# Performance work log

Measured on AMD Instinct MI355X. Metric: run time of the kernel, lower is better.

Reference implementation:

```python
import jax, jax.numpy as jnp
import numpy as np

B, N, F_IN, H, E, C = 64, 1024, 128, 128, 1048576, 6
RATIO = 0.5
N1 = int(N * RATIO)        # nodes per graph after pool1 = 512
N2 = int(N1 * RATIO)       # nodes per graph after pool2 = 256


def setup_inputs() -> dict:
    key = jax.random.key(0)
    ks = jax.random.split(key, 14)
    x = jax.random.normal(ks[0], (B * N, F_IN), jnp.float32)
    # edges constrained within each graph (uniform graph size N)
    src = jax.random.randint(ks[1], (E,), 0, B * N, dtype=jnp.int32)
    dst = (src // N) * N + jax.random.randint(ks[2], (E,), 0, N, dtype=jnp.int32)
    edge_index = jnp.stack([src, dst]).astype(jnp.int64)
    batch = jnp.repeat(jnp.arange(B, dtype=jnp.int64), N)

    def lin(k, i, o):
        return (jax.random.normal(k, (i, o), jnp.float32) / np.sqrt(i)).astype(jnp.float32)

    W1 = lin(ks[3], F_IN, H); b1 = jnp.zeros((H,), jnp.float32)
    ws1 = jax.random.normal(ks[4], (H,), jnp.float32) / np.sqrt(H)
    W2 = lin(ks[5], H, H); b2 = jnp.zeros((H,), jnp.float32)
    ws2 = jax.random.normal(ks[6], (H,), jnp.float32) / np.sqrt(H)
    W3 = lin(ks[7], H, H); b3 = jnp.zeros((H,), jnp.float32)
    ws3 = jax.random.normal(ks[8], (H,), jnp.float32) / np.sqrt(H)
    L1w = lin(ks[9], 2 * H, H); L1b = jnp.zeros((H,), jnp.float32)
    L2w = lin(ks[10], H, H // 2); L2b = jnp.zeros((H // 2,), jnp.float32)
    L3w = lin(ks[11], H // 2, C); L3b = jnp.zeros((C,), jnp.float32)
    return dict(x=x, edge_index=edge_index, batch=batch,
                W1=W1, b1=b1, ws1=ws1, W2=W2, b2=b2, ws2=ws2, W3=W3, b3=b3, ws3=ws3,
                L1w=L1w, L1b=L1b, L2w=L2w, L2b=L2b, L3w=L3w, L3b=L3b)


def gcn_conv(x, src, dst, emask, W, b, ws, n_nodes):
    # GCNConv with self-loops: out_i = sum_j m_ij h_j / sqrt(d_i d_j) + h_i / d_i, d = deg+1
    h = x @ W
    deg = jax.ops.segment_sum(emask, dst, num_segments=n_nodes) + 1.0
    norm = emask / jnp.sqrt(deg[src] * deg[dst])                 # [E]
    agg = jax.ops.segment_sum(h[src] * norm[:, None], dst, num_segments=n_nodes)
    out = agg + h / deg[:, None] + b
    score = out @ ws                                             # [n] attention score
    return out, score


def att_pool(x, score, src, dst, emask, n_per_graph):
    # top-k node selection per graph (uniform sizes -> static shapes)
    k = int(n_per_graph * RATIO)
    vals, idx = jax.lax.top_k(score.reshape(B, n_per_graph), k)  # [B, k]
    gidx = (idx + (jnp.arange(B) * n_per_graph)[:, None]).reshape(-1)
    x_new = x[gidx] * jnp.tanh(vals.reshape(-1))[:, None]
    # remap old node ids -> new compact ids; drop edges touching removed nodes
    newpos = jnp.full((B * n_per_graph,), -1, jnp.int32).at[gidx].set(
        jnp.arange(B * k, dtype=jnp.int32))
    nsrc = newpos[src]; ndst = newpos[dst]
    nmask = emask * (nsrc >= 0) * (ndst >= 0)
    return x_new, jnp.maximum(nsrc, 0), jnp.maximum(ndst, 0), nmask, k


def readout(h, bvec, n_per_graph):
    gmp = jax.ops.segment_max(h, bvec, num_segments=B)
    gap = jax.ops.segment_sum(h, bvec, num_segments=B) / n_per_graph
    return jnp.concatenate([gmp, gap], axis=1)                   # [B, 2H]


def reference(x, edge_index, batch, W1, b1, ws1, W2, b2, ws2, W3, b3, ws3,
              L1w, L1b, L2w, L2b, L3w, L3b):
    src = edge_index[0].astype(jnp.int32)
    dst = edge_index[1].astype(jnp.int32)
    emask = jnp.ones((E,), x.dtype)

    h, s = gcn_conv(x, src, dst, emask, W1, b1, ws1, B * N)
    h = jax.nn.relu(h)
    h, src, dst, emask, k1 = att_pool(h, s, src, dst, emask, N)
    b1v = jnp.repeat(jnp.arange(B), k1)
    x1 = readout(h, b1v, float(k1))

    h, s = gcn_conv(h, src, dst, emask, W2, b2, ws2, B * k1)
    h = jax.nn.relu(h)
    h, src, dst, emask, k2 = att_pool(h, s, src, dst, emask, k1)
    b2v = jnp.repeat(jnp.arange(B), k2)
    x2 = readout(h, b2v, float(k2))

    h, s = gcn_conv(h, src, dst, emask, W3, b3, ws3, B * k2)
    h = jax.nn.relu(h)
    x3 = readout(h, b2v, float(k2))

    z = jax.nn.relu(x1) + jax.nn.relu(x2) + jax.nn.relu(x3)
    z = jax.nn.relu(z @ L1w + L1b)
    z = jax.nn.relu(z @ L2w + L2b)
    return jax.nn.log_softmax(z @ L3w + L3b, axis=-1)
```

## Files before the change

kernel.cpp:

```cpp
#include <hip/hip_runtime.h>
#include <math.h>

#define E_TOT 1048576
#define NB    64
#define HD    128
#define NN1   65536
#define NN2   32768
#define NN3   16384
#define CAP   18432
#define WST   140
#define PSTR  64
#define SMEM_PREP (2*16*128*4 + 2*16*WST*4)

__global__ void probe_kernel(const int* __restrict__ ei, int* __restrict__ flag,
                             int* __restrict__ gcur, int2* __restrict__ csr2) {
    int t = threadIdx.x;
    if (t < 64) { gcur[t] = 0; csr2[E_TOT + t] = make_int2(0, 0); }
    if (blockIdx.x == 0 && t == 0) {
        int w = 1;
        for (int i = 1; i < 64; i += 2) if (ei[i] != 0) { w = 0; break; }
        *flag = w;
    }
}

__device__ __forceinline__ void bin_pack_body(char* smem, const int* __restrict__ ei,
                                              const int* __restrict__ wflag,
                                              int* __restrict__ bins,
                                              int* __restrict__ gcur, int bid) {
    int* hist  = (int*)smem;
    int* base  = hist + 64;
    int* gpos  = base + 64;
    int* stage = gpos + 64;
    const int t = threadIdx.x;
    const int wide = *wflag;
    const int e0 = bid * 4096;
    const int2* ei2 = (const int2*)ei;

    int pk[16];
    #pragma unroll
    for (int j = 0; j < 16; ++j) {
        int e = e0 + j * 256 + t;
        int s, d;
        if (wide) { s = ei2[e].x; d = ei2[E_TOT + e].x; }
        else      { s = ei[e];    d = ei[E_TOT + e]; }
        int g = d >> 10;
        pk[j] = (g << 20) | ((d & 1023) << 10) | (s & 1023);
    }
    if (t < 64) hist[t] = 0;
    __syncthreads();
    #pragma unroll
    for (int j = 0; j < 16; ++j) atomicAdd(&hist[pk[j] >> 20], 1);
    __syncthreads();
    if (t < 64) {
        int v = hist[t];
        int inc = v;
        #pragma unroll
        for (int d = 1; d < 64; d <<= 1) { int u = __shfl_up(inc, d); if (t >= d) inc += u; }
        base[t] = inc - v;
        gpos[t] = atomicAdd(&gcur[t], v);
    }
    __syncthreads();
    if (t < 64) hist[t] = base[t];
    __syncthreads();
    #pragma unroll
    for (int j = 0; j < 16; ++j) {
        int p = atomicAdd(&hist[pk[j] >> 20], 1);
        stage[p] = pk[j];
    }
    __syncthreads();
    #pragma unroll
    for (int j = 0; j < 16; ++j) {
        int i = j * 256 + t;
        int v = stage[i];
        int g = v >> 20;
        int dst = gpos[g] + (i - base[g]);
        if (dst < CAP) bins[g * CAP + dst] = v;
    }
}

__device__ __forceinline__ void gemm_body(char* smem, const float* __restrict__ X,
                                          const int* __restrict__ sel,
                                          const float* __restrict__ scal,
                                          const float* __restrict__ W,
                                          float* __restrict__ Y, int bid) {
    float* sXT = (float*)smem;
    float* sW  = sXT + 2 * 16 * 128;
    const int t = threadIdx.x;
    const long long row0 = (long long)bid * 128;
    const int r0 = (t >> 4) << 3;
    const int c0 = (t & 15) << 3;
    const int wofs = c0 + ((c0 >> 5) << 2);
    const int lm  = t >> 1;
    const int lk  = (t & 1) << 3;
    const int wk  = t >> 4;
    const int wc8 = (t & 15) << 3;
    const int wpos = wc8 + ((wc8 >> 5) << 2);

    const float* xrow;
    float sc;
    if (sel) { xrow = X + (long long)sel[row0 + lm] * 128; sc = scal[row0 + lm]; }
    else     { xrow = X + (row0 + lm) * 128;               sc = 1.f; }

    float acc[8][8];
    #pragma unroll
    for (int i = 0; i < 8; ++i)
        #pragma unroll
        for (int j = 0; j < 8; ++j) acc[i][j] = 0.f;

    {
        float4 xa = *(const float4*)(xrow + lk);
        float4 xb = *(const float4*)(xrow + lk + 4);
        float4 wa = *(const float4*)(W + wk * 128 + wc8);
        float4 wb = *(const float4*)(W + wk * 128 + wc8 + 4);
        sXT[(lk + 0) * 128 + lm] = xa.x * sc; sXT[(lk + 1) * 128 + lm] = xa.y * sc;
        sXT[(lk + 2) * 128 + lm] = xa.z * sc; sXT[(lk + 3) * 128 + lm] = xa.w * sc;
        sXT[(lk + 4) * 128 + lm] = xb.x * sc; sXT[(lk + 5) * 128 + lm] = xb.y * sc;
        sXT[(lk + 6) * 128 + lm] = xb.z * sc; sXT[(lk + 7) * 128 + lm] = xb.w * sc;
        *(float4*)&sW[wk * WST + wpos]     = wa;
        *(float4*)&sW[wk * WST + wpos + 4] = wb;
    }
    int cur = 0;
    for (int k0 = 0; k0 < 128; k0 += 16) {
        __syncthreads();
        const bool hasNext = (k0 + 16) < 128;
        float4 nxa, nxb, nwa, nwb;
        if (hasNext) {
            nxa = *(const float4*)(xrow + k0 + 16 + lk);
            nxb = *(const float4*)(xrow + k0 + 16 + lk + 4);
            nwa = *(const float4*)(W + (k0 + 16 + wk) * 128 + wc8);
            nwb = *(const float4*)(W + (k0 + 16 + wk) * 128 + wc8 + 4);
        }
        #pragma unroll
        for (int kk = 0; kk < 16; ++kk) {
            float4 xa = *(const float4*)&sXT[(cur * 16 + kk) * 128 + r0];
            float4 xb = *(const float4*)&sXT[(cur * 16 + kk) * 128 + r0 + 4];
            float4 wa = *(const float4*)&sW[(cur * 16 + kk) * WST + wofs];
            float4 wb = *(const float4*)&sW[(cur * 16 + kk) * WST + wofs + 4];
            float xr[8]  = {xa.x, xa.y, xa.z, xa.w, xb.x, xb.y, xb.z, xb.w};
            float wcv[8] = {wa.x, wa.y, wa.z, wa.w, wb.x, wb.y, wb.z, wb.w};
            #pragma unroll
            for (int i = 0; i < 8; ++i)
                #pragma unroll
                for (int j = 0; j < 8; ++j)
                    acc[i][j] = fmaf(xr[i], wcv[j], acc[i][j]);
        }
        if (hasNext) {
            int nxt = cur ^ 1;
            sXT[(nxt * 16 + lk + 0) * 128 + lm] = nxa.x * sc;
            sXT[(nxt * 16 + lk + 1) * 128 + lm] = nxa.y * sc;
            sXT[(nxt * 16 + lk + 2) * 128 + lm] = nxa.z * sc;
            sXT[(nxt * 16 + lk + 3) * 128 + lm] = nxa.w * sc;
            sXT[(nxt * 16 + lk + 4) * 128 + lm] = nxb.x * sc;
            sXT[(nxt * 16 + lk + 5) * 128 + lm] = nxb.y * sc;
            sXT[(nxt * 16 + lk + 6) * 128 + lm] = nxb.z * sc;
            sXT[(nxt * 16 + lk + 7) * 128 + lm] = nxb.w * sc;
            *(float4*)&sW[(nxt * 16 + wk) * WST + wpos]     = nwa;
            *(float4*)&sW[(nxt * 16 + wk) * WST + wpos + 4] = nwb;
            cur = nxt;
        }
    }

    #pragma unroll
    for (int i = 0; i < 8; ++i) {
        float* yp = Y + (row0 + r0 + i) * 128 + c0;
        float4 o0; o0.x = acc[i][0]; o0.y = acc[i][1]; o0.z = acc[i][2]; o0.w = acc[i][3];
        float4 o1; o1.x = acc[i][4]; o1.y = acc[i][5]; o1.z = acc[i][6]; o1.w = acc[i][7];
        *(float4*)yp       = o0;
        *(float4*)(yp + 4) = o1;
    }
}

__device__ __forceinline__ void csr_build_body(const int2* __restrict__ old_off2,
                                               const int* __restrict__ old_deg,
                                               const int* __restrict__ old_csr,
                                               int old_stride,
                                               const int* __restrict__ map,
                                               const int* __restrict__ sel,
                                               int* __restrict__ new_csr,
                                               int* __restrict__ deg,
                                               float* __restrict__ rs,
                                               int nnew, int wid, int lane) {
    if (wid >= nnew) return;
    int old = sel[wid];
    int beg, end;
    if (old_off2) { int2 oe = old_off2[old]; beg = oe.x; end = oe.y; }
    else          { beg = old * PSTR; end = beg + old_deg[old]; }
    int out = wid * PSTR;
    int total = 0;
    for (int base = beg; base < end; base += 64) {
        int i = base + lane;
        int ns = -1;
        if (i < end) ns = map[old_csr[i * old_stride]];
        unsigned long long b = __ballot(ns >= 0);
        int pos = __popcll(b & ((1ULL << lane) - 1));
        if (ns >= 0 && total + pos < PSTR) new_csr[out + total + pos] = ns;
        total += __popcll(b);
    }
    if (total > PSTR) total = PSTR;
    if (lane == 0) {
        deg[wid] = total;
        rs[wid]  = rsqrtf((float)(total + 1));
    }
}

__device__ __forceinline__ void readout_g_body(const float* __restrict__ h,
                                               const int* __restrict__ sel,
                                               const float* __restrict__ scal,
                                               float* __restrict__ part,
                                               int npg, int b, int f) {
    int g = b >> 3, c = b & 7;
    int chunk = npg >> 3;
    int i0 = g * npg + c * chunk;
    float m = -INFINITY, s = 0.f;
    for (int n = 0; n < chunk; ++n) {
        int idx = i0 + n;
        float v = h[(long long)sel[idx] * 128 + f] * scal[idx];
        m = fmaxf(m, v);
        s += v;
    }
    part[(size_t)b * 256 + f]       = m;
    part[(size_t)b * 256 + 128 + f] = s;
}

__global__ __launch_bounds__(256) void prep1_kernel(const int* __restrict__ ei,
                                                    const int* __restrict__ wflag,
                                                    int* __restrict__ bins,
                                                    int* __restrict__ gcur,
                                                    const float* __restrict__ X,
                                                    const float* __restrict__ W1,
                                                    float* __restrict__ A) {
    extern __shared__ __align__(16) char smem[];
    if (blockIdx.x < 256) bin_pack_body(smem, ei, wflag, bins, gcur, blockIdx.x);
    else                  gemm_body(smem, X, nullptr, nullptr, W1, A, blockIdx.x - 256);
}

__global__ __launch_bounds__(256) void stage_prep_kernel(
        const float* __restrict__ Bf, const int* __restrict__ sel,
        const float* __restrict__ scal, const float* __restrict__ W,
        float* __restrict__ A,
        const int2* __restrict__ old_off2, const int* __restrict__ old_deg,
        const int* __restrict__ old_csr, int old_stride,
        const int* __restrict__ map, int* __restrict__ new_csr,
        int* __restrict__ deg, float* __restrict__ rs, int nnew,
        float* __restrict__ part, int npg, int ngemm, int ncsr) {
    extern __shared__ __align__(16) char smem[];
    int b = blockIdx.x;
    if (b < ngemm) { gemm_body(smem, Bf, sel, scal, W, A, b); return; }
    b -= ngemm;
    if (b < ncsr) {
        csr_build_body(old_off2, old_deg, old_csr, old_stride, map, sel,
                       new_csr, deg, rs, nnew, b * 4 + (threadIdx.x >> 6),
                       threadIdx.x & 63);
        return;
    }
    b -= ncsr;
    readout_g_body(Bf, sel, scal, part, npg, b * 2 + (threadIdx.x >> 7),
                   threadIdx.x & 127);
}

__global__ __launch_bounds__(1024) void graph_csr_kernel(const int* __restrict__ bins,
                                                         const int* __restrict__ gcur,
                                                         int2* __restrict__ off2,
                                                         float* __restrict__ rs,
                                                         int2* __restrict__ csr2,
                                                         int* __restrict__ perm) {
    __shared__ int   deg[1024];
    __shared__ int   cur[1024];
    __shared__ float rsl[1024];
    __shared__ int   wsum[16];
    __shared__ int   dh[64];
    __shared__ int   dc[64];
    __shared__ int   ebase_s;
    const int g = blockIdx.x, t = threadIdx.x;
    const int lane = t & 63, wv = t >> 6;

    if (t < 64) {
        int v = gcur[t];
        int inc = v;
        #pragma unroll
        for (int d = 1; d < 64; d <<= 1) { int u = __shfl_up(inc, d); if (t >= d) inc += u; }
        if (t == g) ebase_s = inc - v;
    }
    deg[t] = 0;
    if (t < 64) dh[t] = 0;
    __syncthreads();
    const int cnt = gcur[g];
    const int ebase = ebase_s;
    const int* bin = bins + g * CAP;

    for (int i = t; i < cnt; i += 1024)
        atomicAdd(&deg[(bin[i] >> 10) & 1023], 1);
    __syncthreads();

    int dv = deg[t];
    int dcap = dv < 63 ? dv : 63;
    atomicAdd(&dh[dcap], 1);
    int inc = dv;
    #pragma unroll
    for (int d = 1; d < 64; d <<= 1) { int u = __shfl_up(inc, d); if (lane >= d) inc += u; }
    if (lane == 63) wsum[wv] = inc;
    __syncthreads();
    if (t < 16) {
        int v = wsum[t];
        int inc2 = v;
        #pragma unroll
        for (int d = 1; d < 16; d <<= 1) { int u = __shfl_up(inc2, d); if (t >= d) inc2 += u; }
        wsum[t] = inc2 - v;
    }
    if (t >= 64 && t < 128) {
        int l2 = t - 64;
        int v2 = dh[l2];
        int inc3 = v2;
        #pragma unroll
        for (int d = 1; d < 64; d <<= 1) { int u = __shfl_up(inc3, d); if (l2 >= d) inc3 += u; }
        dc[l2] = inc3 - v2;
    }
    __syncthreads();
    int ex = inc - dv + wsum[wv];
    int beg = ebase + ex;
    off2[g * 1024 + t] = make_int2(beg, beg + dv);
    float rv = rsqrtf((float)(dv + 1));
    rs[g * 1024 + t] = rv;
    rsl[t] = rv;
    cur[t] = ex;
    int r2 = atomicAdd(&dc[dcap], 1);
    perm[g * 1024 + r2] = t;
    __syncthreads();

    for (int i = t; i < cnt; i += 1024) {
        int v = bin[i];
        int s = v & 1023;
        int d = (v >> 10) & 1023;
        int p = atomicAdd(&cur[d], 1);
        csr2[ebase + p] = make_int2((g << 10) + s, __float_as_int(rsl[s] * rsl[d]));
    }
}

__global__ __launch_bounds__(1024) void agg_lds_kernel(const float* __restrict__ h,
                                                       const int2* __restrict__ csr2,
                                                       const int2* __restrict__ off2,
                                                       const float* __restrict__ rs,
                                                       const int* __restrict__ perm,
                                                       const float* __restrict__ bias,
                                                       const float* __restrict__ ws,
                                                       float* __restrict__ hrelu,
                                                       float* __restrict__ P) {
    __shared__ float sh[1024 * 36];
    const int t  = threadIdx.x;
    const int g  = blockIdx.x & 63;
    const int fc = blockIdx.x >> 6;
    const int nbase = g << 10;
    const float* hg = h + (size_t)nbase * 128 + fc * 32;

    #pragma unroll
    for (int it = 0; it < 8; ++it) {
        int i = it * 1024 + t;
        int r = i >> 3, p = i & 7;
        float4 v4 = *(const float4*)(hg + (size_t)r * 128 + p * 4);
        *(float4*)&sh[r * 36 + p * 4] = v4;
    }
    __syncthreads();

    const int q   = t & 7;
    const int grp = t >> 3;
    const int qb  = q << 2;

    float4 bb = *(const float4*)(bias + fc * 32 + qb);
    float4 ww = *(const float4*)(ws   + fc * 32 + qb);

    for (int pass = 0; pass < 8; ++pass) {
        int lv = perm[nbase + pass * 128 + grp];
        int v  = nbase + lv;
        int2 oe = off2[v];
        int beg = oe.x, end = oe.y;
        float rv = rs[v];
        float a0 = 0.f, a1 = 0.f, a2 = 0.f, a3 = 0.f;

        int eb = beg;
        for (; eb + 8 <= end; eb += 8) {
            #pragma unroll
            for (int j = 0; j < 8; ++j) {
                int2 e = csr2[eb + j];
                float nj = __int_as_float(e.y);
                const float4 hv4 = *(const float4*)&sh[(e.x & 1023) * 36 + qb];
                a0 = fmaf(hv4.x, nj, a0); a1 = fmaf(hv4.y, nj, a1);
                a2 = fmaf(hv4.z, nj, a2); a3 = fmaf(hv4.w, nj, a3);
            }
        }
        if (eb < end) {
            #pragma unroll
            for (int j = 0; j < 8; ++j) {
                int2 e = csr2[eb + j];
                float nj = (eb + j < end) ? __int_as_float(e.y) : 0.f;
                const float4 hv4 = *(const float4*)&sh[(e.x & 1023) * 36 + qb];
                a0 = fmaf(hv4.x, nj, a0); a1 = fmaf(hv4.y, nj, a1);
                a2 = fmaf(hv4.z, nj, a2); a3 = fmaf(hv4.w, nj, a3);
            }
        }

        float4 hv = *(const float4*)&sh[lv * 36 + qb];
        float inv = rv * rv;
        float o0 = a0 + hv.x * inv + bb.x;
        float o1 = a1 + hv.y * inv + bb.y;
        float o2 = a2 + hv.z * inv + bb.z;
        float o3 = a3 + hv.w * inv + bb.w;

        float pa = o0 * ww.x + o1 * ww.y;
        float pb = o2 * ww.z + o3 * ww.w;
        *(float2*)(P + (size_t)v * 64 + (fc * 8 + q) * 2) = make_float2(pa, pb);

        float4 o;
        o.x = fmaxf(o0, 0.f); o.y = fmaxf(o1, 0.f);
        o.z = fmaxf(o2, 0.f); o.w = fmaxf(o3, 0.f);
        *(float4*)(hrelu + (size_t)v * 128 + fc * 32 + qb) = o;
    }
}

__global__ __launch_bounds__(256) void score1_kernel(const float* __restrict__ P,
                                                     float* __restrict__ score) {
    int v = blockIdx.x * 256 + threadIdx.x;
    const float* buf = P + (size_t)v * 64;
    float a[32], b[32];
    #pragma unroll
    for (int i2 = 0; i2 < 16; ++i2) {
        float4 v4 = *(const float4*)(buf + i2 * 4);
        a[i2 * 2]     = v4.x; b[i2 * 2]     = v4.y;
        a[i2 * 2 + 1] = v4.z; b[i2 * 2 + 1] = v4.w;
    }
    float ua[16], ub[16];
    #pragma unroll
    for (int l = 0; l < 16; ++l) { ua[l] = a[l] + a[l + 16]; ub[l] = b[l] + b[l + 16]; }
    float va[8], vb[8];
    #pragma unroll
    for (int l = 0; l < 8; ++l) { va[l] = ua[l] + ua[l + 8]; vb[l] = ub[l] + ub[l + 8]; }
    float wa[4], wb[4];
    #pragma unroll
    for (int l = 0; l < 4; ++l) { wa[l] = va[l] + va[l + 4]; wb[l] = vb[l] + vb[l + 4]; }
    float xa0 = wa[0] + wa[2], xa1 = wa[1] + wa[3];
    float xb0 = wb[0] + wb[2], xb1 = wb[1] + wb[3];
    score[v] = (xa0 + xa1) + (xb0 + xb1);
}

__global__ __launch_bounds__(256) void agg_kernel(const float* __restrict__ h,
                                                  const int* __restrict__ csr,
                                                  const int2* __restrict__ off2,
                                                  const int* __restrict__ degp,
                                                  const float* __restrict__ rs,
                                                  const float* __restrict__ bias,
                                                  const float* __restrict__ ws,
                                                  float* __restrict__ hrelu,
                                                  float* __restrict__ score,
                                                  int npg, int lbshift, int padded) {
    const int lane = threadIdx.x & 63;
    const int wvb  = threadIdx.x >> 6;
    const int half = lane >> 5;
    const int li   = lane & 31;
    int b   = blockIdx.x;
    int xcd = b & 7;
    int i   = b >> 3;
    int gi  = i >> lbshift;
    int lb  = i & ((1 << lbshift) - 1);
    int g   = xcd + (gi << 3);
    int v   = g * npg + (lb << 3) + (wvb << 1) + half;

    int beg, end;
    if (padded) { beg = v * PSTR; end = beg + degp[v]; }
    else        { int2 oe = off2[v]; beg = oe.x; end = oe.y; }
    float rv = rs[v];
    const float4* h4 = (const float4*)h;
    float ax = 0.f, ay = 0.f, az = 0.f, aw = 0.f;

    for (int base = beg; base < end; base += 32) {
        int idx = base + li;
        int sv = (idx < end) ? csr[idx] : 0;
        int m = end - base; if (m > 32) m = 32;
        int j = 0;
        for (; j + 8 <= m; j += 8) {
            int s0 = __shfl(sv, j,     32);
            int s1 = __shfl(sv, j + 1, 32);
            int s2 = __shfl(sv, j + 2, 32);
            int s3 = __shfl(sv, j + 3, 32);
            int s4 = __shfl(sv, j + 4, 32);
            int s5 = __shfl(sv, j + 5, 32);
            int s6 = __shfl(sv, j + 6, 32);
            int s7 = __shfl(sv, j + 7, 32);
            float n0 = rs[s0] * rv, n1 = rs[s1] * rv, n2 = rs[s2] * rv, n3 = rs[s3] * rv;
            float n4 = rs[s4] * rv, n5 = rs[s5] * rv, n6 = rs[s6] * rv, n7 = rs[s7] * rv;
            float4 v0 = h4[(long long)s0 * 32 + li];
            float4 v1 = h4[(long long)s1 * 32 + li];
            float4 v2 = h4[(long long)s2 * 32 + li];
            float4 v3 = h4[(long long)s3 * 32 + li];
            float4 v4 = h4[(long long)s4 * 32 + li];
            float4 v5 = h4[(long long)s5 * 32 + li];
            float4 v6 = h4[(long long)s6 * 32 + li];
            float4 v7 = h4[(long long)s7 * 32 + li];
            ax = fmaf(v0.x, n0, ax); ay = fmaf(v0.y, n0, ay); az = fmaf(v0.z, n0, az); aw = fmaf(v0.w, n0, aw);
            ax = fmaf(v1.x, n1, ax); ay = fmaf(v1.y, n1, ay); az = fmaf(v1.z, n1, az); aw = fmaf(v1.w, n1, aw);
            ax = fmaf(v2.x, n2, ax); ay = fmaf(v2.y, n2, ay); az = fmaf(v2.z, n2, az); aw = fmaf(v2.w, n2, aw);
            ax = fmaf(v3.x, n3, ax); ay = fmaf(v3.y, n3, ay); az = fmaf(v3.z, n3, az); aw = fmaf(v3.w, n3, aw);
            ax = fmaf(v4.x, n4, ax); ay = fmaf(v4.y, n4, ay); az = fmaf(v4.z, n4, az); aw = fmaf(v4.w, n4, aw);
            ax = fmaf(v5.x, n5, ax); ay = fmaf(v5.y, n5, ay); az = fmaf(v5.z, n5, az); aw = fmaf(v5.w, n5, aw);
            ax = fmaf(v6.x, n6, ax); ay = fmaf(v6.y, n6, ay); az = fmaf(v6.z, n6, az); aw = fmaf(v6.w, n6, aw);
            ax = fmaf(v7.x, n7, ax); ay = fmaf(v7.y, n7, ay); az = fmaf(v7.z, n7, az); aw = fmaf(v7.w, n7, aw);
        }
        for (; j < m; ++j) {
            int s = __shfl(sv, j, 32);
            float n = rs[s] * rv;
            float4 vv = h4[(long long)s * 32 + li];
            ax = fmaf(vv.x, n, ax); ay = fmaf(vv.y, n, ay);
            az = fmaf(vv.z, n, az); aw = fmaf(vv.w, n, aw);
        }
    }

    float4 hv = h4[(long long)v * 32 + li];
    float inv = rv * rv;
    float4 bb = ((const float4*)bias)[li];
    float4 ww = ((const float4*)ws)[li];
    float o0 = ax + hv.x * inv + bb.x;
    float o1 = ay + hv.y * inv + bb.y;
    float o2 = az + hv.z * inv + bb.z;
    float o3 = aw + hv.w * inv + bb.w;

    float pa = o0 * ww.x + o1 * ww.y;
    float pb = o2 * ww.z + o3 * ww.w;
    #pragma unroll
    for (int dd = 16; dd; dd >>= 1) {
        pa += __shfl_xor(pa, dd, 32);
        pb += __shfl_xor(pb, dd, 32);
    }
    float p = pa + pb;
    if (li == 0) score[v] = p;

    float4 o;
    o.x = fmaxf(o0, 0.f); o.y = fmaxf(o1, 0.f);
    o.z = fmaxf(o2, 0.f); o.w = fmaxf(o3, 0.f);
    ((float4*)hrelu)[(long long)v * 32 + li] = o;
}

__global__ __launch_bounds__(1024) void topk_kernel(const float* __restrict__ score,
                                                    int* __restrict__ newpos,
                                                    int* __restrict__ sel,
                                                    float* __restrict__ scale,
                                                    int n, int k) {
    __shared__ float key[1024];
    __shared__ int   kid[1024];
    int g = blockIdx.x, t = threadIdx.x;
    key[t] = score[g * n + t];
    kid[t] = t;
    __syncthreads();
    for (int kk = 2; kk <= n; kk <<= 1) {
        for (int j = kk >> 1; j > 0; j >>= 1) {
            int ixj = t ^ j;
            if (ixj > t) {
                bool dir = ((t & kk) == 0);
                float a = key[t], b = key[ixj];
                if ((a < b) == dir) {
                    key[t] = b; key[ixj] = a;
                    int tmp = kid[t]; kid[t] = kid[ixj]; kid[ixj] = tmp;
                }
            }
            __syncthreads();
        }
    }
    int old = g * n + kid[t];
    if (t < k) {
        int nid = g * k + t;
        newpos[old] = nid;
        sel[nid]    = old;
        scale[nid]  = tanhf(key[t]);
    } else {
        newpos[old] = -1;
    }
}

__global__ __launch_bounds__(128) void readout_part_kernel(const float* __restrict__ h,
                                                           float* __restrict__ part, int npg) {
    int b = blockIdx.x;
    int g = b >> 3, c = b & 7;
    int f = threadIdx.x;
    int chunk = npg >> 3;
    const float* base = h + ((long long)g * npg + (long long)c * chunk) * 128;
    float m = -INFINITY, s = 0.f;
    for (int n = 0; n < chunk; ++n) {
        float v = base[n * 128 + f];
        m = fmaxf(m, v);
        s += v;
    }
    part[(size_t)b * 256 + f]       = m;
    part[(size_t)b * 256 + 128 + f] = s;
}

__global__ __launch_bounds__(128) void mlp_kernel(const float* __restrict__ part1,
                                                  const float* __restrict__ part2,
                                                  const float* __restrict__ part3,
                                                  const float* __restrict__ L1w,
                                                  const float* __restrict__ L1b,
                                                  const float* __restrict__ L2w,
                                                  const float* __restrict__ L2b,
                                                  const float* __restrict__ L3w,
                                                  const float* __restrict__ L3b,
                                                  float* __restrict__ out) {
    __shared__ float z[256], z1[128], z2[64], z3[6];
    int g = blockIdx.x, t = threadIdx.x;
    float m1 = -INFINITY, s1 = 0.f, m2 = -INFINITY, s2 = 0.f, m3 = -INFINITY, s3 = 0.f;
    #pragma unroll
    for (int c = 0; c < 8; ++c) {
        size_t o = (size_t)(g * 8 + c) * 256;
        m1 = fmaxf(m1, part1[o + t]); s1 += part1[o + 128 + t];
        m2 = fmaxf(m2, part2[o + t]); s2 += part2[o + 128 + t];
        m3 = fmaxf(m3, part3[o + t]); s3 += part3[o + 128 + t];
    }
    z[t]       = fmaxf(m1, 0.f) + fmaxf(m2, 0.f) + fmaxf(m3, 0.f);
    z[t + 128] = fmaxf(s1 / 512.f, 0.f) + fmaxf(s2 / 256.f, 0.f) + fmaxf(s3 / 256.f, 0.f);
    __syncthreads();
    float a = L1b[t];
    for (int i = 0; i < 256; ++i) a += z[i] * L1w[i * 128 + t];
    z1[t] = fmaxf(a, 0.f);
    __syncthreads();
    if (t < 64) {
        float b = L2b[t];
        for (int i = 0; i < 128; ++i) b += z1[i] * L2w[i * 64 + t];
        z2[t] = fmaxf(b, 0.f);
    }
    __syncthreads();
    if (t < 6) {
        float c = L3b[t];
        for (int i = 0; i < 64; ++i) c += z2[i] * L3w[i * 6 + t];
        z3[t] = c;
    }
    __syncthreads();
    if (t == 0) {
        float m = z3[0];
        for (int i = 1; i < 6; ++i) m = fmaxf(m, z3[i]);
        float s = 0.f;
        for (int i = 0; i < 6; ++i) s += expf(z3[i] - m);
        float ls = m + logf(s);
        for (int i = 0; i < 6; ++i) out[g * 6 + i] = z3[i] - ls;
    }
}

extern "C" void kernel_launch(void* const* d_in, const int* in_sizes, int n_in,
                              void* d_out, int out_size, void* d_ws, size_t ws_size,
                              hipStream_t stream) {
    const float* x    = (const float*)d_in[0];
    const int*   ei   = (const int*)d_in[1];
    const float* W1   = (const float*)d_in[3];
    const float* b1   = (const float*)d_in[4];
    const float* ws1  = (const float*)d_in[5];
    const float* W2   = (const float*)d_in[6];
    const float* b2   = (const float*)d_in[7];
    const float* ws2  = (const float*)d_in[8];
    const float* W3   = (const float*)d_in[9];
    const float* b3   = (const float*)d_in[10];
    const float* ws3  = (const float*)d_in[11];
    const float* L1w  = (const float*)d_in[12];
    const float* L1b  = (const float*)d_in[13];
    const float* L2w  = (const float*)d_in[14];
    const float* L2b  = (const float*)d_in[15];
    const float* L3w  = (const float*)d_in[16];
    const float* L3b  = (const float*)d_in[17];
    float* out = (float*)d_out;

    char* w = (char*)d_ws;
    auto alloc = [&](size_t nbytes) { char* p = w; w += (nbytes + 255) & ~(size_t)255; return p; };
    float* A     = (float*)alloc((size_t)NN1 * 128 * 4);
    float* Bf    = (float*)alloc((size_t)NN1 * 128 * 4);
    float* P1    = (float*)alloc((size_t)NN1 * 64 * 4);
    float* P2    = (float*)alloc((size_t)NN3 * 128 * 4);
    int2*  csr2  = (int2*)alloc((size_t)(E_TOT + 64) * 8);
    int*   degA  = (int*)alloc((size_t)NN2 * 4);
    int*   degB  = (int*)alloc((size_t)NN3 * 4);
    int2*  off2A = (int2*)alloc((size_t)NN1 * 8);
    float* rs    = (float*)alloc((size_t)NN1 * 4);
    int*   perm  = (int*)alloc((size_t)NN1 * 4);
    int*   np1   = (int*)alloc((size_t)NN1 * 4);
    int*   np2   = (int*)alloc((size_t)NN2 * 4);
    int*   sel   = (int*)alloc((size_t)NN2 * 4);
    float* scal  = (float*)alloc((size_t)NN2 * 4);
    float* score = (float*)alloc((size_t)NN1 * 4);
    float* part1 = (float*)alloc((size_t)NB * 8 * 256 * 4);
    float* part2 = (float*)alloc((size_t)NB * 8 * 256 * 4);
    float* part3 = (float*)alloc((size_t)NB * 8 * 256 * 4);
    int*   gcur  = (int*)alloc(64 * 4);
    int*   flag  = (int*)alloc(256);

    int*   bins = (int*)P2;
    float* Pp   = P1;
    int*   csrB = (int*)P1;
    int*   csrC = (int*)csr2;

    probe_kernel<<<1, 64, 0, stream>>>(ei, flag, gcur, csr2);

    prep1_kernel<<<768, 256, SMEM_PREP, stream>>>(ei, flag, bins, gcur, x, W1, A);
    graph_csr_kernel<<<NB, 1024, 0, stream>>>(bins, gcur, off2A, rs, csr2, perm);
    agg_lds_kernel<<<256, 1024, 0, stream>>>(A, csr2, off2A, rs, perm, b1, ws1, Bf, Pp);
    score1_kernel<<<NN1 / 256, 256, 0, stream>>>(Pp, score);
    topk_kernel<<<NB, 1024, 0, stream>>>(score, np1, sel, scal, 1024, 512);

    stage_prep_kernel<<<256 + NN2 / 4 + 256, 256, SMEM_PREP, stream>>>(
        Bf, sel, scal, W2, A, off2A, nullptr, (const int*)csr2, 2,
        np1, csrB, degA, rs, NN2, part1, 512, 256, NN2 / 4);
    agg_kernel<<<NN2 / 8, 256, 0, stream>>>(A, csrB, nullptr, degA, rs, b2, ws2,
                                            Bf, score, 512, 6, 1);
    topk_kernel<<<NB, 512, 0, stream>>>(score, np2, sel, scal, 512, 256);

    stage_prep_kernel<<<128 + NN3 / 4 + 256, 256, SMEM_PREP, stream>>>(
        Bf, sel, scal, W3, A, nullptr, degA, csrB, 1,
        np2, csrC, degB, rs, NN3, part2, 256, 128, NN3 / 4);
    agg_kernel<<<NN3 / 8, 256, 0, stream>>>(A, csrC, nullptr, degB, rs, b3, ws3,
                                            Bf, score, 256, 5, 1);
    readout_part_kernel<<<NB * 8, 128, 0, stream>>>(Bf, part3, 256);

    mlp_kernel<<<NB, 128, 0, stream>>>(part1, part2, part3, L1w, L1b, L2w, L2b,
                                       L3w, L3b, out);
}
```

Baseline: 357.4 us.

## Fuse pooled readout into GEMM staging and split CSR build into own kernel

```diff
diff --git a/kernel.cpp b/kernel.cpp
--- a/kernel.cpp
+++ b/kernel.cpp
@@ -82,7 +82,8 @@
                                           const int* __restrict__ sel,
                                           const float* __restrict__ scal,
                                           const float* __restrict__ W,
-                                          float* __restrict__ Y, int bid) {
+                                          float* __restrict__ Y, int bid,
+                                          float* __restrict__ part, int CH) {
     float* sXT = (float*)smem;
     float* sW  = sXT + 2 * 16 * 128;
     const int t = threadIdx.x;
@@ -122,6 +123,22 @@
     int cur = 0;
     for (int k0 = 0; k0 < 128; k0 += 16) {
         __syncthreads();
+        if (part) {
+            int nu = 2048 / CH;
+            if (t < nu) {
+                int kk = t & 15, ch = t >> 4;
+                const float* col = &sXT[(cur * 16 + kk) * 128 + ch * CH];
+                float m = -INFINITY, s = 0.f;
+                for (int n = 0; n < CH; ++n) {
+                    float v = col[n];
+                    m = fmaxf(m, v);
+                    s += v;
+                }
+                size_t gc = (size_t)bid * (128 / CH) + ch;
+                part[gc * 256 + k0 + kk]       = m;
+                part[gc * 256 + 128 + k0 + kk] = s;
+            }
+        }
         const bool hasNext = (k0 + 16) < 128;
         float4 nxa, nxb, nwa, nwb;
         if (hasNext) {
@@ -170,16 +187,41 @@
     }
 }
 
-__device__ __forceinline__ void csr_build_body(const int2* __restrict__ old_off2,
-                                               const int* __restrict__ old_deg,
-                                               const int* __restrict__ old_csr,
-                                               int old_stride,
-                                               const int* __restrict__ map,
-                                               const int* __restrict__ sel,
-                                               int* __restrict__ new_csr,
-                                               int* __restrict__ deg,
-                                               float* __restrict__ rs,
-                                               int nnew, int wid, int lane) {
+__global__ __launch_bounds__(256) void prep1_kernel(const int* __restrict__ ei,
+                                                    const int* __restrict__ wflag,
+                                                    int* __restrict__ bins,
+                                                    int* __restrict__ gcur,
+                                                    const float* __restrict__ X,
+                                                    const float* __restrict__ W1,
+                                                    float* __restrict__ A) {
+    extern __shared__ __align__(16) char smem[];
+    if (blockIdx.x < 256) bin_pack_body(smem, ei, wflag, bins, gcur, blockIdx.x);
+    else                  gemm_body(smem, X, nullptr, nullptr, W1, A, blockIdx.x - 256,
+                                    nullptr, 64);
+}
+
+__global__ __launch_bounds__(256) void gemm_fused_kernel(const float* __restrict__ Bf,
+                                                         const int* __restrict__ sel,
+                                                         const float* __restrict__ scal,
+                                                         const float* __restrict__ W,
+                                                         float* __restrict__ A,
+                                                         float* __restrict__ part,
+                                                         int CH) {
+    extern __shared__ __align__(16) char smem[];
+    gemm_body(smem, Bf, sel, scal, W, A, blockIdx.x, part, CH);
+}
+
+__global__ __launch_bounds__(256) void csr_build_kernel(const int2* __restrict__ old_off2,
+                                                        const int* __restrict__ old_deg,
+                                                        const int* __restrict__ old_csr,
+                                                        int old_stride,
+                                                        const int* __restrict__ map,
+                                                        const int* __restrict__ sel,
+                                                        int* __restrict__ new_csr,
+                                                        int* __restrict__ deg,
+                                                        float* __restrict__ rs, int nnew) {
+    int wid  = (blockIdx.x * blockDim.x + threadIdx.x) >> 6;
+    int lane = threadIdx.x & 63;
     if (wid >= nnew) return;
     int old = sel[wid];
     int beg, end;
@@ -201,61 +243,6 @@
         deg[wid] = total;
         rs[wid]  = rsqrtf((float)(total + 1));
     }
-}
-
-__device__ __forceinline__ void readout_g_body(const float* __restrict__ h,
-                                               const int* __restrict__ sel,
-                                               const float* __restrict__ scal,
-                                               float* __restrict__ part,
-                                               int npg, int b, int f) {
-    int g = b >> 3, c = b & 7;
-    int chunk = npg >> 3;
-    int i0 = g * npg + c * chunk;
-    float m = -INFINITY, s = 0.f;
-    for (int n = 0; n < chunk; ++n) {
-        int idx = i0 + n;
-        float v = h[(long long)sel[idx] * 128 + f] * scal[idx];
-        m = fmaxf(m, v);
-        s += v;
-    }
-    part[(size_t)b * 256 + f]       = m;
-    part[(size_t)b * 256 + 128 + f] = s;
-}
-
-__global__ __launch_bounds__(256) void prep1_kernel(const int* __restrict__ ei,
-                                                    const int* __restrict__ wflag,
-                                                    int* __restrict__ bins,
-                                                    int* __restrict__ gcur,
-                                                    const float* __restrict__ X,
-                                                    const float* __restrict__ W1,
-                                                    float* __restrict__ A) {
-    extern __shared__ __align__(16) char smem[];
-    if (blockIdx.x < 256) bin_pack_body(smem, ei, wflag, bins, gcur, blockIdx.x);
-    else                  gemm_body(smem, X, nullptr, nullptr, W1, A, blockIdx.x - 256);
-}
-
-__global__ __launch_bounds__(256) void stage_prep_kernel(
-        const float* __restrict__ Bf, const int* __restrict__ sel,
-        const float* __restrict__ scal, const float* __restrict__ W,
-        float* __restrict__ A,
-        const int2* __restrict__ old_off2, const int* __restrict__ old_deg,
-        const int* __restrict__ old_csr, int old_stride,
-        const int* __restrict__ map, int* __restrict__ new_csr,
-        int* __restrict__ deg, float* __restrict__ rs, int nnew,
-        float* __restrict__ part, int npg, int ngemm, int ncsr) {
-    extern __shared__ __align__(16) char smem[];
-    int b = blockIdx.x;
-    if (b < ngemm) { gemm_body(smem, Bf, sel, scal, W, A, b); return; }
-    b -= ngemm;
-    if (b < ncsr) {
-        csr_build_body(old_off2, old_deg, old_csr, old_stride, map, sel,
-                       new_csr, deg, rs, nnew, b * 4 + (threadIdx.x >> 6),
-                       threadIdx.x & 63);
-        return;
-    }
-    b -= ncsr;
-    readout_g_body(Bf, sel, scal, part, npg, b * 2 + (threadIdx.x >> 7),
-                   threadIdx.x & 127);
 }
 
 __global__ __launch_bounds__(1024) void graph_csr_kernel(const int* __restrict__ bins,
@@ -697,16 +684,18 @@
     score1_kernel<<<NN1 / 256, 256, 0, stream>>>(Pp, score);
     topk_kernel<<<NB, 1024, 0, stream>>>(score, np1, sel, scal, 1024, 512);
 
-    stage_prep_kernel<<<256 + NN2 / 4 + 256, 256, SMEM_PREP, stream>>>(
-        Bf, sel, scal, W2, A, off2A, nullptr, (const int*)csr2, 2,
-        np1, csrB, degA, rs, NN2, part1, 512, 256, NN2 / 4);
+    csr_build_kernel<<<NN2 / 4, 256, 0, stream>>>(off2A, nullptr, (const int*)csr2, 2,
+                                                  np1, sel, csrB, degA, rs, NN2);
+    gemm_fused_kernel<<<NN2 / 128, 256, SMEM_PREP, stream>>>(Bf, sel, scal, W2, A,
+                                                             part1, 64);
     agg_kernel<<<NN2 / 8, 256, 0, stream>>>(A, csrB, nullptr, degA, rs, b2, ws2,
                                             Bf, score, 512, 6, 1);
     topk_kernel<<<NB, 512, 0, stream>>>(score, np2, sel, scal, 512, 256);
 
-    stage_prep_kernel<<<128 + NN3 / 4 + 256, 256, SMEM_PREP, stream>>>(
-        Bf, sel, scal, W3, A, nullptr, degA, csrB, 1,
-        np2, csrC, degB, rs, NN3, part2, 256, 128, NN3 / 4);
+    csr_build_kernel<<<NN3 / 4, 256, 0, stream>>>(nullptr, degA, csrB, 1,
+                                                  np2, sel, csrC, degB, rs, NN3);
+    gemm_fused_kernel<<<NN3 / 128, 256, SMEM_PREP, stream>>>(Bf, sel, scal, W3, A,
+                                                             part2, 32);
     agg_kernel<<<NN3 / 8, 256, 0, stream>>>(A, csrC, nullptr, degB, rs, b3, ws3,
                                             Bf, score, 256, 5, 1);
     readout_part_kernel<<<NB * 8, 128, 0, stream>>>(Bf, part3, 256);
```

Result: faster. 336.8 us (-5.8%).
